# Optimization experiments

Measured on AMD Instinct MI355X. Metric: run time of the kernel, lower is better.

## Reference

```python
import jax, jax.numpy as jnp
from jax import lax
import numpy as np

# Layer configuration (from init_kwargs; see FilteringActLayer.__init__)
UP = 2                      # up_factor (temp_rate 32 / in_rate 16)
DOWN = 2                    # down_factor (temp_rate 32 / out_rate 16)
PADDING = (11, 10, 11, 10)  # (px0, px1, py0, py1), derived pad_total = 21
GAIN = float(np.sqrt(2.0))  # lrelu gain used in StyleGAN3
SLOPE = 0.2                 # leaky relu negative slope
CLAMP = 256.0               # activation clamp
UP_TAPS = 12
IN_CUTOFF = 8.0
OUT_CUTOFF = 8.0
IN_HALF_WIDTH = 6.0
OUT_HALF_WIDTH = 6.0
TEMP_FS = 32.0              # max(in_rate, out_rate) * act_upsampling


def _design_lowpass(numtaps, cutoff, width, fs):
    """Replicates scipy.signal.firwin(numtaps, cutoff, width=width, fs=fs)."""
    nyq = fs / 2.0
    # kaiser_atten / kaiser_beta
    atten = 2.285 * (numtaps - 1) * np.pi * (width / nyq) + 7.95
    if atten > 50.0:
        beta = 0.1102 * (atten - 8.7)
    elif atten > 21.0:
        beta = 0.5842 * (atten - 21.0) ** 0.4 + 0.07886 * (atten - 21.0)
    else:
        beta = 0.0
    m = np.arange(numtaps) - (numtaps - 1) / 2.0
    c = cutoff / nyq
    h = c * np.sinc(c * m)
    h = h * np.kaiser(numtaps, beta)
    h = h / np.sum(h)  # unity gain at DC (firwin scale=True)
    return h.astype(np.float32)


def _upfirdn2d_sep(x, f, up, down, pad, gain):
    """Zero-insert upsample by `up`, pad, correlate with separable 1D FIR f
    (applied flipped, i.e. true convolution as in the torch reference),
    then subsample by `down`. x: [N,C,H,W], f: [taps]."""
    N, C, H, W = x.shape
    fr = f[::-1].astype(x.dtype)
    kH = fr.reshape(1, 1, -1, 1)
    kW = fr.reshape(1, 1, 1, -1)
    px0, px1, py0, py1 = pad
    xr = x.reshape(N * C, 1, H, W)
    # lhs_dilation implements the zero-insertion; +up-1 hi-pad accounts for the
    # trailing zeros the torch reference keeps after upsampling.
    xr = lax.conv_general_dilated(xr, kH, window_strides=(down, 1),
                                  padding=((py0, py1 + up - 1), (0, 0)),
                                  lhs_dilation=(up, 1))
    xr = lax.conv_general_dilated(xr, kW, window_strides=(1, down),
                                  padding=((0, 0), (px0, px1 + up - 1)),
                                  lhs_dilation=(1, up))
    Ho, Wo = xr.shape[2], xr.shape[3]
    return xr.reshape(N, C, Ho, Wo) * gain


def setup_inputs() -> dict:
    key = jax.random.key(0)
    k1, k2 = jax.random.split(key)
    x = jax.random.normal(k1, (8, 512, 64, 64), dtype=jnp.float32)
    bias = jax.random.normal(k2, (512,), dtype=jnp.float32) * 0.1
    up_filter = jnp.asarray(_design_lowpass(UP_TAPS, IN_CUTOFF, IN_HALF_WIDTH * 2, TEMP_FS))
    down_filter = jnp.asarray(_design_lowpass(UP_TAPS, OUT_CUTOFF, OUT_HALF_WIDTH * 2, TEMP_FS))
    return {"x": x, "bias": bias, "up_filter": up_filter, "down_filter": down_filter}


def reference(x, bias, up_filter, down_filter):
    # (1) FIR upsample (gain = up^2 to preserve signal magnitude)
    y = _upfirdn2d_sep(x, up_filter, UP, 1, PADDING, float(UP * UP))
    # (2) bias + leaky-relu + gain + clamp (bias_act 'lrelu')
    y = y + bias[None, :, None, None]
    y = jnp.where(y >= 0, y, y * SLOPE) * GAIN
    y = jnp.clip(y, -CLAMP, CLAMP)
    # (3) FIR downsample
    y = _upfirdn2d_sep(y, down_filter, 1, DOWN, (0, 0, 0, 0), 1.0)
    return y
```

## Files before the change

### kernel.cpp

```cpp
#include <hip/hip_runtime.h>

#define SIN 80
#define ST1 80
#define ST3 72

__global__ __launch_bounds__(256, 5)
void synth_fused(const float* __restrict__ x, const float* __restrict__ bias,
                 const float* __restrict__ fu, const float* __restrict__ fd,
                 float* __restrict__ out)
{
    __shared__ __align__(16) float bufA[3024];
    __shared__ __align__(16) float bufB[3376];
    __shared__ float sfilt[24];
    float* const s_in = bufA;
    float* const s_t3 = bufA;
    float* const s_t1 = bufB;

    const int tid  = threadIdx.x;
    const int bx   = blockIdx.x;
    const int tile = bx & 3;
    const int nc   = bx >> 2;
    const int gy0  = tile << 4;

    if (tid < 24) sfilt[tid] = (tid < 12) ? fu[tid] : fd[tid - 12];
    const float bc = bias[nc & 511];
    const float* __restrict__ xc = x + ((size_t)nc << 12);

    #pragma unroll
    for (int it = 0; it < 2; ++it) {
        int idx = tid + it * 256;
        if (idx < 416) {
            int r  = idx >> 4;
            int c4 = (idx & 15) << 2;
            int gy = gy0 - 5 + r;
            float4 v = make_float4(0.f, 0.f, 0.f, 0.f);
            if ((unsigned)gy < 64u)
                v = *reinterpret_cast<const float4*>(xc + (gy << 6) + c4);
            float* dst = s_in + r * SIN + 5 + c4;
            dst[0] = v.x; dst[1] = v.y; dst[2] = v.z; dst[3] = v.w;
        }
    }
    #pragma unroll
    for (int it = 0; it < 2; ++it) {
        int idx = tid + it * 256;
        if (idx < 416) {
            int r  = idx >> 4;
            int pc = idx & 15;
            int c  = (pc < 5) ? pc : (64 + pc);
            s_in[r * SIN + c] = 0.0f;
        }
    }
    __syncthreads();

    float u[12], g[12];
    #pragma unroll
    for (int k = 0; k < 12; ++k) u[k] = sfilt[k];
    #pragma unroll
    for (int k = 0; k < 12; ++k) g[k] = sfilt[23 - k];

    if (tid < 222) {
        const int g3 = tid / 74;
        const int c  = tid - 74 * g3;
        const float* ip = s_in + (7 * g3) * SIN + c;
        float rv[12];
        #pragma unroll
        for (int j = 0; j < 12; ++j) rv[j] = ip[j * SIN];
        float* op = s_t1 + (14 * g3) * ST1 + c;
        #pragma unroll
        for (int m = 0; m < 7; ++m) {
            float aE = u[10]*rv[m];
            aE = fmaf(u[8], rv[m+1], aE); aE = fmaf(u[6], rv[m+2], aE);
            aE = fmaf(u[4], rv[m+3], aE); aE = fmaf(u[2], rv[m+4], aE);
            aE = fmaf(u[0], rv[m+5], aE);
            float aO = u[11]*rv[m];
            aO = fmaf(u[9], rv[m+1], aO); aO = fmaf(u[7], rv[m+2], aO);
            aO = fmaf(u[5], rv[m+3], aO); aO = fmaf(u[3], rv[m+4], aO);
            aO = fmaf(u[1], rv[m+5], aO);
            op[(2*m) * ST1]     = aE;
            op[(2*m + 1) * ST1] = aO;
        }
    }
    __syncthreads();

    #pragma unroll
    for (int k = 0; k < 12; ++k) u[k] *= 4.0f;

    if (tid < 252) {
        const int r = tid / 6;
        const int q = tid - 6 * r;
        const float* t1r = s_t1 + r * ST1 + 12 * q;
        float w[22];
        #pragma unroll
        for (int j = 0; j < 5; ++j) {
            float4 v4 = *reinterpret_cast<const float4*>(t1r + 4 * j);
            w[4*j] = v4.x; w[4*j+1] = v4.y; w[4*j+2] = v4.z; w[4*j+3] = v4.w;
        }
        { float2 v2 = *reinterpret_cast<const float2*>(t1r + 20); w[20] = v2.x; w[21] = v2.y; }
        const float P = 0.84852813742385703f;
        const float Q = 0.56568542494923802f;
        float t2v[34];
        #pragma unroll
        for (int i = 0; i < 17; ++i) {
            float zE = fmaf(u[10], w[i], bc);
            zE = fmaf(u[8], w[i+1], zE); zE = fmaf(u[6], w[i+2], zE);
            zE = fmaf(u[4], w[i+3], zE); zE = fmaf(u[2], w[i+4], zE);
            zE = fmaf(u[0], w[i+5], zE);
            float zO = fmaf(u[11], w[i], bc);
            zO = fmaf(u[9], w[i+1], zO); zO = fmaf(u[7], w[i+2], zO);
            zO = fmaf(u[5], w[i+3], zO); zO = fmaf(u[3], w[i+4], zO);
            zO = fmaf(u[1], w[i+5], zO);
            float vE = fmaf(Q, __builtin_fabsf(zE), P * zE);
            float vO = fmaf(Q, __builtin_fabsf(zO), P * zO);
            t2v[2*i]   = __builtin_amdgcn_fmed3f(vE, -256.0f, 256.0f);
            t2v[2*i+1] = __builtin_amdgcn_fmed3f(vO, -256.0f, 256.0f);
        }
        float* t3r = s_t3 + r * ST3 + 12 * q;
        #pragma unroll
        for (int i = 0; i < 3; ++i) {
            float4 o4;
            float* op = &o4.x;
            #pragma unroll
            for (int s = 0; s < 4; ++s) {
                const int oi = 4 * i + s;
                float acc = g[0] * t2v[2*oi];
                #pragma unroll
                for (int k = 1; k < 12; ++k) acc = fmaf(g[k], t2v[2*oi + k], acc);
                op[s] = acc;
            }
            *reinterpret_cast<float4*>(t3r + 4 * i) = o4;
        }
    }
    __syncthreads();

    {
        const int c  = tid & 63;
        const int rc = tid >> 6;
        const float* t3c = s_t3 + (rc << 3) * ST3 + c;
        float wv[18];
        #pragma unroll
        for (int j = 0; j < 18; ++j) wv[j] = t3c[j * ST3];
        float* op = out + ((size_t)nc << 12) + ((size_t)(gy0 + (rc << 2)) << 6) + c;
        #pragma unroll
        for (int i = 0; i < 4; ++i) {
            float acc = g[0] * wv[2*i];
            #pragma unroll
            for (int k = 1; k < 12; ++k) acc = fmaf(g[k], wv[2*i + k], acc);
            op[(size_t)(i << 6)] = acc;
        }
    }
}

extern "C" void kernel_launch(void* const* d_in, const int* in_sizes, int n_in,
                              void* d_out, int out_size, void* d_ws, size_t ws_size,
                              hipStream_t stream) {
    const float* x    = (const float*)d_in[0];
    const float* bias = (const float*)d_in[1];
    const float* fu   = (const float*)d_in[2];
    const float* fd   = (const float*)d_in[3];
    float* out        = (float*)d_out;

    dim3 grid(8 * 512 * 4);
    dim3 block(256);
    hipLaunchKernelGGL(synth_fused, grid, block, 0, stream, x, bias, fu, fd, out);
}
```

Measured before the change: 154.6 us.

## Double block size to 512 threads and split per-thread work finer

```diff
diff --git a/kernel.cpp b/kernel.cpp
--- a/kernel.cpp
+++ b/kernel.cpp
@@ -4,7 +4,7 @@
 #define ST1 80
 #define ST3 72
 
-__global__ __launch_bounds__(256, 5)
+__global__ __launch_bounds__(512, 8)
 void synth_fused(const float* __restrict__ x, const float* __restrict__ bias,
                  const float* __restrict__ fu, const float* __restrict__ fd,
                  float* __restrict__ out)
@@ -26,29 +26,21 @@
     const float bc = bias[nc & 511];
     const float* __restrict__ xc = x + ((size_t)nc << 12);
 
-    #pragma unroll
-    for (int it = 0; it < 2; ++it) {
-        int idx = tid + it * 256;
-        if (idx < 416) {
-            int r  = idx >> 4;
-            int c4 = (idx & 15) << 2;
-            int gy = gy0 - 5 + r;
-            float4 v = make_float4(0.f, 0.f, 0.f, 0.f);
-            if ((unsigned)gy < 64u)
-                v = *reinterpret_cast<const float4*>(xc + (gy << 6) + c4);
-            float* dst = s_in + r * SIN + 5 + c4;
-            dst[0] = v.x; dst[1] = v.y; dst[2] = v.z; dst[3] = v.w;
-        }
+    if (tid < 416) {
+        int r  = tid >> 4;
+        int c4 = (tid & 15) << 2;
+        int gy = gy0 - 5 + r;
+        float4 v = make_float4(0.f, 0.f, 0.f, 0.f);
+        if ((unsigned)gy < 64u)
+            v = *reinterpret_cast<const float4*>(xc + (gy << 6) + c4);
+        float* dst = s_in + r * SIN + 5 + c4;
+        dst[0] = v.x; dst[1] = v.y; dst[2] = v.z; dst[3] = v.w;
     }
-    #pragma unroll
-    for (int it = 0; it < 2; ++it) {
-        int idx = tid + it * 256;
-        if (idx < 416) {
-            int r  = idx >> 4;
-            int pc = idx & 15;
-            int c  = (pc < 5) ? pc : (64 + pc);
-            s_in[r * SIN + c] = 0.0f;
-        }
+    if (tid < 416) {
+        int r  = tid >> 4;
+        int pc = tid & 15;
+        int c  = (pc < 5) ? pc : (64 + pc);
+        s_in[r * SIN + c] = 0.0f;
     }
     __syncthreads();
 
@@ -58,26 +50,30 @@
     #pragma unroll
     for (int k = 0; k < 12; ++k) g[k] = sfilt[23 - k];
 
-    if (tid < 222) {
-        const int g3 = tid / 74;
-        const int c  = tid - 74 * g3;
-        const float* ip = s_in + (7 * g3) * SIN + c;
-        float rv[12];
-        #pragma unroll
-        for (int j = 0; j < 12; ++j) rv[j] = ip[j * SIN];
-        float* op = s_t1 + (14 * g3) * ST1 + c;
-        #pragma unroll
-        for (int m = 0; m < 7; ++m) {
-            float aE = u[10]*rv[m];
-            aE = fmaf(u[8], rv[m+1], aE); aE = fmaf(u[6], rv[m+2], aE);
-            aE = fmaf(u[4], rv[m+3], aE); aE = fmaf(u[2], rv[m+4], aE);
-            aE = fmaf(u[0], rv[m+5], aE);
-            float aO = u[11]*rv[m];
-            aO = fmaf(u[9], rv[m+1], aO); aO = fmaf(u[7], rv[m+2], aO);
-            aO = fmaf(u[5], rv[m+3], aO); aO = fmaf(u[3], rv[m+4], aO);
-            aO = fmaf(u[1], rv[m+5], aO);
-            op[(2*m) * ST1]     = aE;
-            op[(2*m + 1) * ST1] = aO;
+    #pragma unroll
+    for (int it = 0; it < 2; ++it) {
+        int idx = tid + (it << 9);
+        if (idx < 518) {
+            const int mg = idx / 74;
+            const int c  = idx - 74 * mg;
+            const float* ip = s_in + (3 * mg) * SIN + c;
+            float rv[8];
+            #pragma unroll
+            for (int j = 0; j < 8; ++j) rv[j] = ip[j * SIN];
+            float* op = s_t1 + (6 * mg) * ST1 + c;
+            #pragma unroll
+            for (int m = 0; m < 3; ++m) {
+                float aE = u[10]*rv[m];
+                aE = fmaf(u[8], rv[m+1], aE); aE = fmaf(u[6], rv[m+2], aE);
+                aE = fmaf(u[4], rv[m+3], aE); aE = fmaf(u[2], rv[m+4], aE);
+                aE = fmaf(u[0], rv[m+5], aE);
+                float aO = u[11]*rv[m];
+                aO = fmaf(u[9], rv[m+1], aO); aO = fmaf(u[7], rv[m+2], aO);
+                aO = fmaf(u[5], rv[m+3], aO); aO = fmaf(u[3], rv[m+4], aO);
+                aO = fmaf(u[1], rv[m+5], aO);
+                op[(2*m) * ST1]     = aE;
+                op[(2*m + 1) * ST1] = aO;
+            }
         }
     }
     __syncthreads();
@@ -85,22 +81,21 @@
     #pragma unroll
     for (int k = 0; k < 12; ++k) u[k] *= 4.0f;
 
-    if (tid < 252) {
-        const int r = tid / 6;
-        const int q = tid - 6 * r;
-        const float* t1r = s_t1 + r * ST1 + 12 * q;
-        float w[22];
+    if (tid < 504) {
+        const int r = tid / 12;
+        const int h = tid - 12 * r;
+        const float* t1r = s_t1 + r * ST1 + 6 * h;
+        float w[16];
         #pragma unroll
-        for (int j = 0; j < 5; ++j) {
-            float4 v4 = *reinterpret_cast<const float4*>(t1r + 4 * j);
-            w[4*j] = v4.x; w[4*j+1] = v4.y; w[4*j+2] = v4.z; w[4*j+3] = v4.w;
+        for (int j = 0; j < 8; ++j) {
+            float2 v2 = *reinterpret_cast<const float2*>(t1r + 2 * j);
+            w[2*j] = v2.x; w[2*j+1] = v2.y;
         }
-        { float2 v2 = *reinterpret_cast<const float2*>(t1r + 20); w[20] = v2.x; w[21] = v2.y; }
         const float P = 0.84852813742385703f;
         const float Q = 0.56568542494923802f;
-        float t2v[34];
+        float t2v[22];
         #pragma unroll
-        for (int i = 0; i < 17; ++i) {
+        for (int i = 0; i < 11; ++i) {
             float zE = fmaf(u[10], w[i], bc);
             zE = fmaf(u[8], w[i+1], zE); zE = fmaf(u[6], w[i+2], zE);
             zE = fmaf(u[4], w[i+3], zE); zE = fmaf(u[2], w[i+4], zE);
@@ -114,20 +109,19 @@
             t2v[2*i]   = __builtin_amdgcn_fmed3f(vE, -256.0f, 256.0f);
             t2v[2*i+1] = __builtin_amdgcn_fmed3f(vO, -256.0f, 256.0f);
         }
-        float* t3r = s_t3 + r * ST3 + 12 * q;
+        float* t3r = s_t3 + r * ST3 + 6 * h;
         #pragma unroll
         for (int i = 0; i < 3; ++i) {
-            float4 o4;
-            float* op = &o4.x;
+            float2 o2;
             #pragma unroll
-            for (int s = 0; s < 4; ++s) {
-                const int oi = 4 * i + s;
+            for (int s = 0; s < 2; ++s) {
+                const int oi = 2 * i + s;
                 float acc = g[0] * t2v[2*oi];
                 #pragma unroll
                 for (int k = 1; k < 12; ++k) acc = fmaf(g[k], t2v[2*oi + k], acc);
-                op[s] = acc;
+                (&o2.x)[s] = acc;
             }
-            *reinterpret_cast<float4*>(t3r + 4 * i) = o4;
+            *reinterpret_cast<float2*>(t3r + 2 * i) = o2;
         }
     }
     __syncthreads();
@@ -135,17 +129,17 @@
     {
         const int c  = tid & 63;
         const int rc = tid >> 6;
-        const float* t3c = s_t3 + (rc << 3) * ST3 + c;
-        float wv[18];
+        const float* t3c = s_t3 + (rc << 2) * ST3 + c;
+        float wv[14];
         #pragma unroll
-        for (int j = 0; j < 18; ++j) wv[j] = t3c[j * ST3];
-        float* op = out + ((size_t)nc << 12) + ((size_t)(gy0 + (rc << 2)) << 6) + c;
+        for (int j = 0; j < 14; ++j) wv[j] = t3c[j * ST3];
+        float* op = out + ((size_t)nc << 12) + ((size_t)(gy0 + (rc << 1)) << 6) + c;
         #pragma unroll
-        for (int i = 0; i < 4; ++i) {
-            float acc = g[0] * wv[2*i];
+        for (int s = 0; s < 2; ++s) {
+            float acc = g[0] * wv[2*s];
             #pragma unroll
-            for (int k = 1; k < 12; ++k) acc = fmaf(g[k], wv[2*i + k], acc);
-            op[(size_t)(i << 6)] = acc;
+            for (int k = 1; k < 12; ++k) acc = fmaf(g[k], wv[2*s + k], acc);
+            op[(size_t)(s << 6)] = acc;
         }
     }
 }
@@ -160,6 +154,6 @@
     float* out        = (float*)d_out;
 
     dim3 grid(8 * 512 * 4);
-    dim3 block(256);
+    dim3 block(512);
     hipLaunchKernelGGL(synth_fused, grid, block, 0, stream, x, bias, fu, fd, out);
 }
```

Result: slower. 161.8 us (+4.6%).

## Use packed fp32 FMA for all FIR stages and simplify leaky-relu

Applied to the files above, without the earlier changes.

```diff
diff --git a/kernel.cpp b/kernel.cpp
--- a/kernel.cpp
+++ b/kernel.cpp
@@ -4,7 +4,19 @@
 #define ST1 80
 #define ST3 72
 
-__global__ __launch_bounds__(256, 5)
+typedef float v2f __attribute__((ext_vector_type(2)));
+
+static __device__ __forceinline__ v2f fma2(v2f a, v2f b, v2f c) {
+    return __builtin_elementwise_fma(a, b, c);
+}
+static __device__ __forceinline__ v2f bcast2(float s) {
+    v2f r; r.x = s; r.y = s; return r;
+}
+static __device__ __forceinline__ v2f mk2(float a, float b) {
+    v2f r; r.x = a; r.y = b; return r;
+}
+
+__global__ __launch_bounds__(256, 4)
 void synth_fused(const float* __restrict__ x, const float* __restrict__ bias,
                  const float* __restrict__ fu, const float* __restrict__ fd,
                  float* __restrict__ out)
@@ -52,11 +64,12 @@
     }
     __syncthreads();
 
-    float u[12], g[12];
+    v2f upk[6], gpk[6];
     #pragma unroll
-    for (int k = 0; k < 12; ++k) u[k] = sfilt[k];
-    #pragma unroll
-    for (int k = 0; k < 12; ++k) g[k] = sfilt[23 - k];
+    for (int j = 0; j < 6; ++j) {
+        upk[j] = mk2(sfilt[10 - 2*j], sfilt[11 - 2*j]);
+        gpk[j] = mk2(sfilt[23 - 2*j], sfilt[22 - 2*j]);
+    }
 
     if (tid < 222) {
         const int g3 = tid / 74;
@@ -68,22 +81,21 @@
         float* op = s_t1 + (14 * g3) * ST1 + c;
         #pragma unroll
         for (int m = 0; m < 7; ++m) {
-            float aE = u[10]*rv[m];
-            aE = fmaf(u[8], rv[m+1], aE); aE = fmaf(u[6], rv[m+2], aE);
-            aE = fmaf(u[4], rv[m+3], aE); aE = fmaf(u[2], rv[m+4], aE);
-            aE = fmaf(u[0], rv[m+5], aE);
-            float aO = u[11]*rv[m];
-            aO = fmaf(u[9], rv[m+1], aO); aO = fmaf(u[7], rv[m+2], aO);
-            aO = fmaf(u[5], rv[m+3], aO); aO = fmaf(u[3], rv[m+4], aO);
-            aO = fmaf(u[1], rv[m+5], aO);
-            op[(2*m) * ST1]     = aE;
-            op[(2*m + 1) * ST1] = aO;
+            v2f acc = upk[0] * bcast2(rv[m]);
+            #pragma unroll
+            for (int j = 1; j < 6; ++j)
+                acc = fma2(upk[j], bcast2(rv[m + j]), acc);
+            op[(2*m) * ST1]     = acc.x;
+            op[(2*m + 1) * ST1] = acc.y;
         }
     }
     __syncthreads();
 
+    const float S42 = 4.0f * 1.41421356237309515f;
+    v2f upk2[6];
     #pragma unroll
-    for (int k = 0; k < 12; ++k) u[k] *= 4.0f;
+    for (int j = 0; j < 6; ++j) upk2[j] = upk[j] * S42;
+    const float bcs = bc * 1.41421356237309515f;
 
     if (tid < 252) {
         const int r = tid / 6;
@@ -91,28 +103,21 @@
         const float* t1r = s_t1 + r * ST1 + 12 * q;
         float w[22];
         #pragma unroll
-        for (int j = 0; j < 5; ++j) {
-            float4 v4 = *reinterpret_cast<const float4*>(t1r + 4 * j);
-            w[4*j] = v4.x; w[4*j+1] = v4.y; w[4*j+2] = v4.z; w[4*j+3] = v4.w;
+        for (int j = 0; j < 11; ++j) {
+            v2f v2 = *reinterpret_cast<const v2f*>(t1r + 2 * j);
+            w[2*j] = v2.x; w[2*j+1] = v2.y;
         }
-        { float2 v2 = *reinterpret_cast<const float2*>(t1r + 20); w[20] = v2.x; w[21] = v2.y; }
-        const float P = 0.84852813742385703f;
-        const float Q = 0.56568542494923802f;
-        float t2v[34];
+        const v2f bc2 = bcast2(bcs);
+        v2f t2p[17];
         #pragma unroll
         for (int i = 0; i < 17; ++i) {
-            float zE = fmaf(u[10], w[i], bc);
-            zE = fmaf(u[8], w[i+1], zE); zE = fmaf(u[6], w[i+2], zE);
-            zE = fmaf(u[4], w[i+3], zE); zE = fmaf(u[2], w[i+4], zE);
-            zE = fmaf(u[0], w[i+5], zE);
-            float zO = fmaf(u[11], w[i], bc);
-            zO = fmaf(u[9], w[i+1], zO); zO = fmaf(u[7], w[i+2], zO);
-            zO = fmaf(u[5], w[i+3], zO); zO = fmaf(u[3], w[i+4], zO);
-            zO = fmaf(u[1], w[i+5], zO);
-            float vE = fmaf(Q, __builtin_fabsf(zE), P * zE);
-            float vO = fmaf(Q, __builtin_fabsf(zO), P * zO);
-            t2v[2*i]   = __builtin_amdgcn_fmed3f(vE, -256.0f, 256.0f);
-            t2v[2*i+1] = __builtin_amdgcn_fmed3f(vO, -256.0f, 256.0f);
+            v2f acc = bc2;
+            #pragma unroll
+            for (int j = 0; j < 6; ++j)
+                acc = fma2(upk2[j], bcast2(w[i + j]), acc);
+            v2f mx = __builtin_elementwise_max(acc, acc * 0.2f);
+            t2p[i] = mk2(__builtin_amdgcn_fmed3f(mx.x, -256.0f, 256.0f),
+                         __builtin_amdgcn_fmed3f(mx.y, -256.0f, 256.0f));
         }
         float* t3r = s_t3 + r * ST3 + 12 * q;
         #pragma unroll
@@ -122,10 +127,10 @@
             #pragma unroll
             for (int s = 0; s < 4; ++s) {
                 const int oi = 4 * i + s;
-                float acc = g[0] * t2v[2*oi];
+                v2f acc = gpk[0] * t2p[oi];
                 #pragma unroll
-                for (int k = 1; k < 12; ++k) acc = fmaf(g[k], t2v[2*oi + k], acc);
-                op[s] = acc;
+                for (int j = 1; j < 6; ++j) acc = fma2(gpk[j], t2p[oi + j], acc);
+                op[s] = acc.x + acc.y;
             }
             *reinterpret_cast<float4*>(t3r + 4 * i) = o4;
         }
@@ -136,16 +141,17 @@
         const int c  = tid & 63;
         const int rc = tid >> 6;
         const float* t3c = s_t3 + (rc << 3) * ST3 + c;
-        float wv[18];
+        v2f vp[9];
         #pragma unroll
-        for (int j = 0; j < 18; ++j) wv[j] = t3c[j * ST3];
+        for (int m = 0; m < 9; ++m)
+            vp[m] = mk2(t3c[(2*m) * ST3], t3c[(2*m + 1) * ST3]);
         float* op = out + ((size_t)nc << 12) + ((size_t)(gy0 + (rc << 2)) << 6) + c;
         #pragma unroll
         for (int i = 0; i < 4; ++i) {
-            float acc = g[0] * wv[2*i];
+            v2f acc = gpk[0] * vp[i];
             #pragma unroll
-            for (int k = 1; k < 12; ++k) acc = fmaf(g[k], wv[2*i + k], acc);
-            op[(size_t)(i << 6)] = acc;
+            for (int j = 1; j < 6; ++j) acc = fma2(gpk[j], vp[i + j], acc);
+            op[(size_t)(i << 6)] = acc.x + acc.y;
         }
     }
 }
```

Result: faster. 151.4 us (-2.0%).
